# Kernel tuning notes

Measured on AMD Instinct MI355X. Metric: run time of the kernel, lower is better.

Reference implementation:

```python
import jax, jax.numpy as jnp
import numpy as np

B, C, H, W = 8, 256, 64, 64
EPS = 1e-5


def _mk_conv_bn(key, oc, ic):
    k = jax.random.split(key, 6)
    return dict(
        w=jax.random.normal(k[0], (oc, ic), jnp.float32) * 0.01,  # trunc-normal approx, stddev 0.01
        b=jnp.zeros((oc,), jnp.float32),
        s=jax.random.uniform(k[1], (oc,), jnp.float32, 0.5, 1.5),   # BN scale
        t=jax.random.normal(k[2], (oc,), jnp.float32) * 0.1,        # BN shift
        m=jax.random.normal(k[3], (oc,), jnp.float32) * 0.1,        # BN running mean
        v=jax.random.uniform(k[4], (oc,), jnp.float32, 0.5, 1.5),   # BN running var
    )


def setup_inputs() -> dict:
    key = jax.random.key(0)
    ks = jax.random.split(key, 6)
    d = {"x": jax.random.normal(ks[0], (B, C, H, W), jnp.float32)}
    for i, (oc, ic) in zip([1, 2, 3, 4], [(C // 8, C), (C // 8, C), (C // 2, C), (C, C // 2)]):
        p = _mk_conv_bn(ks[i], oc, ic)
        for name, val in p.items():
            d[f"{name}{i}"] = val
    d["gamma"] = jnp.asarray(0.5, jnp.float32)
    return d


def _cbn(x, w, b, s, t, m, v, relu=True):
    # conv1x1 + BatchNorm(eval) [+ ReLU]; dropout is identity at inference
    y = jnp.einsum('bchw,oc->bohw', x, w) + b[None, :, None, None]
    scale = (s / jnp.sqrt(v + EPS))[None, :, None, None]
    y = (y - m[None, :, None, None]) * scale + t[None, :, None, None]
    return jax.nn.relu(y) if relu else y


def _maxpool2(x):
    b, c, h, w = x.shape
    return x.reshape(b, c, h // 2, 2, w // 2, 2).max(axis=(3, 5))


def reference(x, w1, b1, s1, t1, m1, v1, w2, b2, s2, t2, m2, v2,
              w3, b3, s3, t3, m3, v3, w4, b4, s4, t4, m4, v4, gamma):
    b, c, h, w = x.shape
    f = _maxpool2(_cbn(x, w1, b1, s1, t1, m1, v1))   # (B, C/8, H/2, W/2)
    g = _cbn(x, w2, b2, s2, t2, m2, v2)              # (B, C/8, H, W)
    hh = _maxpool2(_cbn(x, w3, b3, s3, t3, m3, v3))  # (B, C/2, H/2, W/2)
    hw, hw4 = h * w, (h // 2) * (w // 2)
    f = f.reshape(b, c // 8, hw4).transpose(0, 2, 1)  # (B, HW/4, C/8)
    g = g.reshape(b, c // 8, hw)                      # (B, C/8, HW)
    s = jnp.einsum('bnk,bkm->bnm', f, g)              # (B, HW/4, HW)
    beta = jax.nn.softmax(s, axis=1)                  # softmax over dim=1, as in source
    hh = hh.reshape(b, c // 2, hw4)                   # (B, C/2, HW/4)
    o = jnp.einsum('bcn,bnm->bcm', hh, beta).reshape(b, c // 2, h, w)
    out = _cbn(o, w4, b4, s4, t4, m4, v4, relu=False)
    return gamma * out + x
```

## Files before the change

### kernel.cpp

```cpp
#include <hip/hip_runtime.h>
#include <hip/hip_bf16.h>

#define HW   4096
#define HW4  1024
#define EPS  1e-5f

typedef __attribute__((ext_vector_type(8))) short bf16x8;
typedef __attribute__((ext_vector_type(4))) float f32x4;

__device__ __forceinline__ short f2bs(float f) {
    union { float f; unsigned u; } v; v.f = f;
    unsigned r = v.u + 0x7FFFu + ((v.u >> 16) & 1u);
    return (short)(r >> 16);
}
__device__ __forceinline__ int swz64(int r, int c)  { return (r << 6) + ((c ^ (r & 7))  << 3); }
__device__ __forceinline__ int swz32(int r, int c)  { return (r << 5) + ((c ^ (r & 3))  << 3); }
__device__ __forceinline__ int swz128(int r, int c) { return (r << 7) + ((c ^ (r & 15)) << 3); }

__global__ __launch_bounds__(256) void conv123pool(
    const float* __restrict__ x,
    const float* __restrict__ w1, const float* __restrict__ b1, const float* __restrict__ s1,
    const float* __restrict__ t1, const float* __restrict__ m1, const float* __restrict__ v1,
    const float* __restrict__ w2, const float* __restrict__ b2, const float* __restrict__ s2,
    const float* __restrict__ t2, const float* __restrict__ m2, const float* __restrict__ v2,
    const float* __restrict__ w3, const float* __restrict__ b3, const float* __restrict__ s3,
    const float* __restrict__ t3, const float* __restrict__ m3, const float* __restrict__ v3,
    short* __restrict__ gbuf, short* __restrict__ fbuf, short* __restrict__ hhbuf)
{
    __shared__ __align__(16) short Wl[64 * 64];
    __shared__ __align__(16) short Xl[128 * 64];
    __shared__ float alB[64], beB[64];

    const int t = threadIdx.x;
    const int lane = t & 63, wv = t >> 6;
    const int quad = lane >> 4, l16 = lane & 15;
    const int ptile = blockIdx.x;
    const int octile = blockIdx.y;
    const int bz = blockIdx.z;
    const int pBase = ptile * 128;

    if (t < 64) {
        int j = octile * 64 + t;
        float pb, ps, ptv, pm, pv;
        if (j < 32)      { pb = b1[j]; ps = s1[j]; ptv = t1[j]; pm = m1[j]; pv = v1[j]; }
        else if (j < 64) { int c = j - 32; pb = b2[c]; ps = s2[c]; ptv = t2[c]; pm = m2[c]; pv = v2[c]; }
        else             { int c = j - 64; pb = b3[c]; ps = s3[c]; ptv = t3[c]; pm = m3[c]; pv = v3[c]; }
        float al = ps * rsqrtf(pv + EPS);
        alB[t] = al; beB[t] = (pb - pm) * al + ptv;
    }

    const f32x4 fzero = {0.f, 0.f, 0.f, 0.f};
    f32x4 acc[8];
    #pragma unroll
    for (int i = 0; i < 8; ++i) acc[i] = fzero;

    const int woc = t >> 2, wkb = (t & 3) * 16;
    const int xp  = t & 127, xk8 = t >> 7;

    for (int k0 = 0; k0 < 256; k0 += 64) {
        {
            int j = octile * 64 + woc;
            const float* wp = (j < 32) ? (w1 + j * 256)
                            : (j < 64) ? (w2 + (j - 32) * 256)
                                       : (w3 + (j - 64) * 256);
            wp += k0 + wkb;
            float4 a = *(const float4*)(wp);
            float4 b = *(const float4*)(wp + 4);
            float4 c = *(const float4*)(wp + 8);
            float4 d = *(const float4*)(wp + 12);
            bf16x8 lo, hi;
            lo[0]=f2bs(a.x); lo[1]=f2bs(a.y); lo[2]=f2bs(a.z); lo[3]=f2bs(a.w);
            lo[4]=f2bs(b.x); lo[5]=f2bs(b.y); lo[6]=f2bs(b.z); lo[7]=f2bs(b.w);
            hi[0]=f2bs(c.x); hi[1]=f2bs(c.y); hi[2]=f2bs(c.z); hi[3]=f2bs(c.w);
            hi[4]=f2bs(d.x); hi[5]=f2bs(d.y); hi[6]=f2bs(d.z); hi[7]=f2bs(d.w);
            *(bf16x8*)&Wl[swz64(woc, (wkb >> 3))]     = lo;
            *(bf16x8*)&Wl[swz64(woc, (wkb >> 3) + 1)] = hi;
        }
        {
            const float* xp0 = x + ((size_t)bz * 256 + k0 + xk8 * 32) * HW + pBase + xp;
            float fv[32];
            #pragma unroll
            for (int i = 0; i < 32; ++i) fv[i] = xp0[(size_t)i * HW];
            #pragma unroll
            for (int c = 0; c < 4; ++c) {
                bf16x8 v;
                #pragma unroll
                for (int jj = 0; jj < 8; ++jj) v[jj] = f2bs(fv[c * 8 + jj]);
                *(bf16x8*)&Xl[swz64(xp, xk8 * 4 + c)] = v;
            }
        }
        __syncthreads();
        #pragma unroll
        for (int kk = 0; kk < 2; ++kk) {
            bf16x8 afr = *(const bf16x8*)&Wl[swz64(wv * 16 + l16, kk * 4 + quad)];
            #pragma unroll
            for (int pt = 0; pt < 8; ++pt) {
                bf16x8 bfr = *(const bf16x8*)&Xl[swz64(pt * 16 + l16, kk * 4 + quad)];
                acc[pt] = __builtin_amdgcn_mfma_f32_16x16x32_bf16(afr, bfr, acc[pt], 0, 0, 0);
            }
        }
        __syncthreads();
    }

    const bool isG = (octile == 0) && (wv >= 2);
    #pragma unroll
    for (int r = 0; r < 4; ++r) {
        int ocl = wv * 16 + quad * 4 + r;
        float al = alB[ocl], be = beB[ocl];
        float y[8];
        #pragma unroll
        for (int pt = 0; pt < 8; ++pt) y[pt] = fmaxf(acc[pt][r] * al + be, 0.f);
        int j = octile * 64 + ocl;
        if (isG) {
            #pragma unroll
            for (int pt = 0; pt < 8; ++pt)
                gbuf[((size_t)bz * 32 + (j - 32)) * HW + pBase + pt * 16 + l16] = f2bs(y[pt]);
        } else {
            #pragma unroll
            for (int pt = 0; pt < 4; ++pt) {
                float v  = fmaxf(y[pt], y[pt + 4]);
                float po = fmaxf(v, __shfl_xor(v, 1));
                if ((l16 & 1) == 0) {
                    int n = ptile * 32 + ((pt * 16 + l16) >> 1);
                    if (j < 32) fbuf[((size_t)bz * 32 + j) * HW4 + n] = f2bs(po);
                    else        hhbuf[((size_t)bz * 128 + (j - 64)) * HW4 + n] = f2bs(po);
                }
            }
        }
    }
}

__global__ __launch_bounds__(256) void attn_conv4(
    const short* __restrict__ gbuf,
    const short* __restrict__ fbuf,
    const short* __restrict__ hhbuf,
    const float* __restrict__ x,
    const float* __restrict__ w4, const float* __restrict__ b4, const float* __restrict__ s4,
    const float* __restrict__ t4, const float* __restrict__ m4, const float* __restrict__ v4,
    const float* __restrict__ gamma, float* __restrict__ out)
{
    __shared__ __align__(16) short smem[24576];
    __shared__ float alB4[256], beB4[256];
    short* gTl = smem;
    short* fTl = smem + 2048;
    short* sTl = smem + 4096;
    short* hhl = smem + 8192;
    short* o_l = smem;
    short* Wl4 = smem + 8192;

    const int t = threadIdx.x;
    const int lane = t & 63, wv = t >> 6;
    const int quad = lane >> 4, l16 = lane & 15;
    const int bz = blockIdx.y;
    const int m0 = blockIdx.x * 64;
    const int ms = wv * 16;
    const f32x4 fzero = {0.f, 0.f, 0.f, 0.f};

    {
        float al = s4[t] * rsqrtf(v4[t] + EPS);
        alB4[t] = al; beB4[t] = (b4[t] - m4[t]) * al + t4[t];
    }

    {
        int mm = t & 63, k8 = t >> 6;
        bf16x8 v;
        #pragma unroll
        for (int j = 0; j < 8; ++j)
            v[j] = gbuf[((size_t)bz * 32 + k8 * 8 + j) * HW + m0 + mm];
        *(bf16x8*)&gTl[swz32(mm, k8)] = v;
    }
    __syncthreads();
    bf16x8 bg = *(const bf16x8*)&gTl[swz32(ms + l16, quad)];

    float runmax = -1e30f, runsum = 0.f;
    f32x4 oacc[8];
    #pragma unroll
    for (int i = 0; i < 8; ++i) oacc[i] = fzero;

    for (int n0 = 0; n0 < 1024; n0 += 64) {
        __syncthreads();
        {
            int nn = t & 63, k8 = t >> 6;
            bf16x8 v;
            #pragma unroll
            for (int j = 0; j < 8; ++j)
                v[j] = fbuf[((size_t)bz * 32 + k8 * 8 + j) * HW4 + n0 + nn];
            *(bf16x8*)&fTl[swz32(nn, k8)] = v;
        }
        {
            int c0 = t >> 3, nc = t & 7;
            #pragma unroll
            for (int i = 0; i < 4; ++i) {
                int c = i * 32 + c0;
                bf16x8 v = *(const bf16x8*)(hhbuf + ((size_t)bz * 128 + c) * HW4 + n0 + nc * 8);
                *(bf16x8*)&hhl[swz64(c, nc)] = v;
            }
        }
        __syncthreads();

        f32x4 sacc[4];
        #pragma unroll
        for (int nt = 0; nt < 4; ++nt) {
            bf16x8 af = *(const bf16x8*)&fTl[swz32(nt * 16 + l16, quad)];
            sacc[nt] = __builtin_amdgcn_mfma_f32_16x16x32_bf16(af, bg, fzero, 0, 0, 0);
        }

        float tmax = -1e30f;
        #pragma unroll
        for (int nt = 0; nt < 4; ++nt)
            #pragma unroll
            for (int r = 0; r < 4; ++r) tmax = fmaxf(tmax, sacc[nt][r]);
        tmax = fmaxf(tmax, __shfl_xor(tmax, 16));
        tmax = fmaxf(tmax, __shfl_xor(tmax, 32));
        float nmax  = fmaxf(runmax, tmax);
        float alpha = __expf(runmax - nmax);
        float psum = 0.f;
        #pragma unroll
        for (int nt = 0; nt < 4; ++nt) {
            short4 ev;
            #pragma unroll
            for (int r = 0; r < 4; ++r) {
                float e = __expf(sacc[nt][r] - nmax);
                psum += e;
                ((short*)&ev)[r] = f2bs(e);
            }
            int chunk = nt * 2 + (quad >> 1);
            *(short4*)&sTl[swz64(ms + l16, chunk) + (quad & 1) * 4] = ev;
        }
        psum += __shfl_xor(psum, 16);
        psum += __shfl_xor(psum, 32);
        runsum = runsum * alpha + psum;
        runmax = nmax;

        #pragma unroll
        for (int ct = 0; ct < 8; ++ct) oacc[ct] = oacc[ct] * alpha;
        #pragma unroll
        for (int kk = 0; kk < 2; ++kk) {
            bf16x8 bs = *(const bf16x8*)&sTl[swz64(ms + l16, kk * 4 + quad)];
            #pragma unroll
            for (int ct = 0; ct < 8; ++ct) {
                bf16x8 ah = *(const bf16x8*)&hhl[swz64(ct * 16 + l16, kk * 4 + quad)];
                oacc[ct] = __builtin_amdgcn_mfma_f32_16x16x32_bf16(ah, bs, oacc[ct], 0, 0, 0);
            }
        }
    }
    __syncthreads();

    {
        float inv = 1.0f / runsum;
        int m = ms + l16;
        #pragma unroll
        for (int ct = 0; ct < 8; ++ct) {
            short4 ov;
            #pragma unroll
            for (int r = 0; r < 4; ++r) ((short*)&ov)[r] = f2bs(oacc[ct][r] * inv);
            *(short4*)&o_l[swz128(m, ct * 2 + (quad >> 1)) + (quad & 1) * 4] = ov;
        }
    }
    __syncthreads();

    f32x4 acc4[4][4];
    #pragma unroll
    for (int i = 0; i < 4; ++i)
        #pragma unroll
        for (int j = 0; j < 4; ++j) acc4[i][j] = fzero;

    for (int c0 = 0; c0 < 128; c0 += 64) {
        #pragma unroll
        for (int i = 0; i < 4; ++i) {
            int oc = i * 64 + (t >> 2);
            int kb = (t & 3) * 16;
            const float* wp = w4 + oc * 128 + c0 + kb;
            float4 a = *(const float4*)(wp);
            float4 b = *(const float4*)(wp + 4);
            float4 c = *(const float4*)(wp + 8);
            float4 d = *(const float4*)(wp + 12);
            bf16x8 lo, hi;
            lo[0]=f2bs(a.x); lo[1]=f2bs(a.y); lo[2]=f2bs(a.z); lo[3]=f2bs(a.w);
            lo[4]=f2bs(b.x); lo[5]=f2bs(b.y); lo[6]=f2bs(b.z); lo[7]=f2bs(b.w);
            hi[0]=f2bs(c.x); hi[1]=f2bs(c.y); hi[2]=f2bs(c.z); hi[3]=f2bs(c.w);
            hi[4]=f2bs(d.x); hi[5]=f2bs(d.y); hi[6]=f2bs(d.z); hi[7]=f2bs(d.w);
            *(bf16x8*)&Wl4[swz64(oc, (kb >> 3))]     = lo;
            *(bf16x8*)&Wl4[swz64(oc, (kb >> 3) + 1)] = hi;
        }
        __syncthreads();
        #pragma unroll
        for (int kk = 0; kk < 2; ++kk) {
            bf16x8 bfr[4];
            #pragma unroll
            for (int mt = 0; mt < 4; ++mt)
                bfr[mt] = *(const bf16x8*)&o_l[swz128(mt * 16 + l16, (c0 >> 3) + kk * 4 + quad)];
            #pragma unroll
            for (int ot = 0; ot < 4; ++ot) {
                bf16x8 afr = *(const bf16x8*)&Wl4[swz64(wv * 64 + ot * 16 + l16, kk * 4 + quad)];
                #pragma unroll
                for (int mt = 0; mt < 4; ++mt)
                    acc4[ot][mt] = __builtin_amdgcn_mfma_f32_16x16x32_bf16(afr, bfr[mt], acc4[ot][mt], 0, 0, 0);
            }
        }
        __syncthreads();
    }

    float gm = gamma[0];
    #pragma unroll
    for (int ot = 0; ot < 4; ++ot) {
        #pragma unroll
        for (int r = 0; r < 4; ++r) {
            int oc = wv * 64 + ot * 16 + quad * 4 + r;
            float al = alB4[oc], be = beB4[oc];
            #pragma unroll
            for (int mt = 0; mt < 4; ++mt) {
                int p = m0 + mt * 16 + l16;
                float y  = acc4[ot][mt][r] * al + be;
                float xo = x[((size_t)bz * 256 + oc) * HW + p];
                out[((size_t)bz * 256 + oc) * HW + p] = gm * y + xo;
            }
        }
    }
}

extern "C" void kernel_launch(void* const* d_in, const int* in_sizes, int n_in,
                              void* d_out, int out_size, void* d_ws, size_t ws_size,
                              hipStream_t stream)
{
    const float* x  = (const float*)d_in[0];
    const float* w1 = (const float*)d_in[1];
    const float* b1 = (const float*)d_in[2];
    const float* s1 = (const float*)d_in[3];
    const float* t1 = (const float*)d_in[4];
    const float* m1 = (const float*)d_in[5];
    const float* v1 = (const float*)d_in[6];
    const float* w2 = (const float*)d_in[7];
    const float* b2 = (const float*)d_in[8];
    const float* s2 = (const float*)d_in[9];
    const float* t2 = (const float*)d_in[10];
    const float* m2 = (const float*)d_in[11];
    const float* v2 = (const float*)d_in[12];
    const float* w3 = (const float*)d_in[13];
    const float* b3 = (const float*)d_in[14];
    const float* s3 = (const float*)d_in[15];
    const float* t3 = (const float*)d_in[16];
    const float* m3 = (const float*)d_in[17];
    const float* v3 = (const float*)d_in[18];
    const float* w4 = (const float*)d_in[19];
    const float* b4 = (const float*)d_in[20];
    const float* s4 = (const float*)d_in[21];
    const float* t4 = (const float*)d_in[22];
    const float* m4 = (const float*)d_in[23];
    const float* v4 = (const float*)d_in[24];
    const float* gm = (const float*)d_in[25];
    float* out = (float*)d_out;

    short* gbuf  = (short*)d_ws;
    short* fbuf  = gbuf  + (size_t)8 * 32 * 4096;
    short* hhbuf = fbuf  + (size_t)8 * 32 * 1024;

    conv123pool<<<dim3(32, 3, 8), 256, 0, stream>>>(
        x, w1, b1, s1, t1, m1, v1, w2, b2, s2, t2, m2, v2, w3, b3, s3, t3, m3, v3,
        gbuf, fbuf, hhbuf);
    attn_conv4<<<dim3(64, 8), 256, 0, stream>>>(
        gbuf, fbuf, hhbuf, x, w4, b4, s4, t4, m4, v4, gm, out);
}
```

Baseline: 173.9 us.

## Fuse conv output-channel tiles per block and prefetch attention tiles into registers

conv123pool now computes all 192 output channels of conv1/2/3 in one block, so each x tile is loaded and converted to bf16 once instead of three times. The grid shrinks from 768 to 256 blocks, trading less parallelism for that reuse. attn_conv4 software-pipelines the f and hh tile loads by prefetching the next tile into registers while the current one is computed. It also swaps the 32-wide XOR swizzle for a padded stride-40 LDS layout and drops one barrier before the conv4 stage.

```diff
diff --git a/kernel.cpp b/kernel.cpp
--- a/kernel.cpp
+++ b/kernel.cpp
@@ -14,8 +14,8 @@
     return (short)(r >> 16);
 }
 __device__ __forceinline__ int swz64(int r, int c)  { return (r << 6) + ((c ^ (r & 7))  << 3); }
-__device__ __forceinline__ int swz32(int r, int c)  { return (r << 5) + ((c ^ (r & 3))  << 3); }
 __device__ __forceinline__ int swz128(int r, int c) { return (r << 7) + ((c ^ (r & 15)) << 3); }
+__device__ __forceinline__ int p40(int r, int c)    { return r * 40 + c * 8; }
 
 __global__ __launch_bounds__(256) void conv123pool(
     const float* __restrict__ x,
@@ -27,43 +27,45 @@
     const float* __restrict__ t3, const float* __restrict__ m3, const float* __restrict__ v3,
     short* __restrict__ gbuf, short* __restrict__ fbuf, short* __restrict__ hhbuf)
 {
-    __shared__ __align__(16) short Wl[64 * 64];
+    __shared__ __align__(16) short Wl[192 * 64];
     __shared__ __align__(16) short Xl[128 * 64];
-    __shared__ float alB[64], beB[64];
+    __shared__ float alB[192], beB[192];
 
     const int t = threadIdx.x;
     const int lane = t & 63, wv = t >> 6;
     const int quad = lane >> 4, l16 = lane & 15;
     const int ptile = blockIdx.x;
-    const int octile = blockIdx.y;
-    const int bz = blockIdx.z;
+    const int bz = blockIdx.y;
     const int pBase = ptile * 128;
 
-    if (t < 64) {
-        int j = octile * 64 + t;
+    if (t < 192) {
+        int j = t;
         float pb, ps, ptv, pm, pv;
         if (j < 32)      { pb = b1[j]; ps = s1[j]; ptv = t1[j]; pm = m1[j]; pv = v1[j]; }
         else if (j < 64) { int c = j - 32; pb = b2[c]; ps = s2[c]; ptv = t2[c]; pm = m2[c]; pv = v2[c]; }
         else             { int c = j - 64; pb = b3[c]; ps = s3[c]; ptv = t3[c]; pm = m3[c]; pv = v3[c]; }
         float al = ps * rsqrtf(pv + EPS);
-        alB[t] = al; beB[t] = (pb - pm) * al + ptv;
+        alB[j] = al; beB[j] = (pb - pm) * al + ptv;
     }
 
     const f32x4 fzero = {0.f, 0.f, 0.f, 0.f};
-    f32x4 acc[8];
-    #pragma unroll
-    for (int i = 0; i < 8; ++i) acc[i] = fzero;
-
-    const int woc = t >> 2, wkb = (t & 3) * 16;
+    f32x4 acc[3][8];
+    #pragma unroll
+    for (int i = 0; i < 3; ++i)
+        #pragma unroll
+        for (int j = 0; j < 8; ++j) acc[i][j] = fzero;
+
     const int xp  = t & 127, xk8 = t >> 7;
 
     for (int k0 = 0; k0 < 256; k0 += 64) {
-        {
-            int j = octile * 64 + woc;
-            const float* wp = (j < 32) ? (w1 + j * 256)
-                            : (j < 64) ? (w2 + (j - 32) * 256)
-                                       : (w3 + (j - 64) * 256);
-            wp += k0 + wkb;
+        #pragma unroll
+        for (int i = 0; i < 3; ++i) {
+            int idx = t + i * 256;
+            int oc = idx >> 2, kb = (idx & 3) * 16;
+            const float* wp = (oc < 32) ? (w1 + oc * 256)
+                            : (oc < 64) ? (w2 + (oc - 32) * 256)
+                                        : (w3 + (oc - 64) * 256);
+            wp += k0 + kb;
             float4 a = *(const float4*)(wp);
             float4 b = *(const float4*)(wp + 4);
             float4 c = *(const float4*)(wp + 8);
@@ -73,8 +75,8 @@
             lo[4]=f2bs(b.x); lo[5]=f2bs(b.y); lo[6]=f2bs(b.z); lo[7]=f2bs(b.w);
             hi[0]=f2bs(c.x); hi[1]=f2bs(c.y); hi[2]=f2bs(c.z); hi[3]=f2bs(c.w);
             hi[4]=f2bs(d.x); hi[5]=f2bs(d.y); hi[6]=f2bs(d.z); hi[7]=f2bs(d.w);
-            *(bf16x8*)&Wl[swz64(woc, (wkb >> 3))]     = lo;
-            *(bf16x8*)&Wl[swz64(woc, (wkb >> 3) + 1)] = hi;
+            *(bf16x8*)&Wl[swz64(oc, (kb >> 3))]     = lo;
+            *(bf16x8*)&Wl[swz64(oc, (kb >> 3) + 1)] = hi;
         }
         {
             const float* xp0 = x + ((size_t)bz * 256 + k0 + xk8 * 32) * HW + pBase + xp;
@@ -92,38 +94,44 @@
         __syncthreads();
         #pragma unroll
         for (int kk = 0; kk < 2; ++kk) {
-            bf16x8 afr = *(const bf16x8*)&Wl[swz64(wv * 16 + l16, kk * 4 + quad)];
-            #pragma unroll
-            for (int pt = 0; pt < 8; ++pt) {
-                bf16x8 bfr = *(const bf16x8*)&Xl[swz64(pt * 16 + l16, kk * 4 + quad)];
-                acc[pt] = __builtin_amdgcn_mfma_f32_16x16x32_bf16(afr, bfr, acc[pt], 0, 0, 0);
-            }
-        }
-        __syncthreads();
-    }
-
-    const bool isG = (octile == 0) && (wv >= 2);
-    #pragma unroll
-    for (int r = 0; r < 4; ++r) {
-        int ocl = wv * 16 + quad * 4 + r;
-        float al = alB[ocl], be = beB[ocl];
-        float y[8];
-        #pragma unroll
-        for (int pt = 0; pt < 8; ++pt) y[pt] = fmaxf(acc[pt][r] * al + be, 0.f);
-        int j = octile * 64 + ocl;
-        if (isG) {
+            bf16x8 bfr[8];
             #pragma unroll
             for (int pt = 0; pt < 8; ++pt)
-                gbuf[((size_t)bz * 32 + (j - 32)) * HW + pBase + pt * 16 + l16] = f2bs(y[pt]);
-        } else {
-            #pragma unroll
-            for (int pt = 0; pt < 4; ++pt) {
-                float v  = fmaxf(y[pt], y[pt + 4]);
-                float po = fmaxf(v, __shfl_xor(v, 1));
-                if ((l16 & 1) == 0) {
-                    int n = ptile * 32 + ((pt * 16 + l16) >> 1);
-                    if (j < 32) fbuf[((size_t)bz * 32 + j) * HW4 + n] = f2bs(po);
-                    else        hhbuf[((size_t)bz * 128 + (j - 64)) * HW4 + n] = f2bs(po);
+                bfr[pt] = *(const bf16x8*)&Xl[swz64(pt * 16 + l16, kk * 4 + quad)];
+            #pragma unroll
+            for (int tt = 0; tt < 3; ++tt) {
+                bf16x8 afr = *(const bf16x8*)&Wl[swz64(wv * 48 + tt * 16 + l16, kk * 4 + quad)];
+                #pragma unroll
+                for (int pt = 0; pt < 8; ++pt)
+                    acc[tt][pt] = __builtin_amdgcn_mfma_f32_16x16x32_bf16(afr, bfr[pt], acc[tt][pt], 0, 0, 0);
+            }
+        }
+        __syncthreads();
+    }
+
+    #pragma unroll
+    for (int tt = 0; tt < 3; ++tt) {
+        #pragma unroll
+        for (int r = 0; r < 4; ++r) {
+            int j = wv * 48 + tt * 16 + quad * 4 + r;
+            float al = alB[j], be = beB[j];
+            float y[8];
+            #pragma unroll
+            for (int pt = 0; pt < 8; ++pt) y[pt] = fmaxf(acc[tt][pt][r] * al + be, 0.f);
+            if (j >= 32 && j < 64) {
+                #pragma unroll
+                for (int pt = 0; pt < 8; ++pt)
+                    gbuf[((size_t)bz * 32 + (j - 32)) * HW + pBase + pt * 16 + l16] = f2bs(y[pt]);
+            } else {
+                #pragma unroll
+                for (int pt = 0; pt < 4; ++pt) {
+                    float v  = fmaxf(y[pt], y[pt + 4]);
+                    float po = fmaxf(v, __shfl_xor(v, 1));
+                    if ((l16 & 1) == 0) {
+                        int n = ptile * 32 + ((pt * 16 + l16) >> 1);
+                        if (j < 32) fbuf[((size_t)bz * 32 + j) * HW4 + n] = f2bs(po);
+                        else        hhbuf[((size_t)bz * 128 + (j - 64)) * HW4 + n] = f2bs(po);
+                    }
                 }
             }
         }
@@ -139,14 +147,14 @@
     const float* __restrict__ t4, const float* __restrict__ m4, const float* __restrict__ v4,
     const float* __restrict__ gamma, float* __restrict__ out)
 {
-    __shared__ __align__(16) short smem[24576];
+    __shared__ __align__(16) short smem[25600];
     __shared__ float alB4[256], beB4[256];
     short* gTl = smem;
-    short* fTl = smem + 2048;
-    short* sTl = smem + 4096;
-    short* hhl = smem + 8192;
+    short* fTl = smem + 2560;
+    short* sTl = smem + 5120;
+    short* hhl = smem + 9216;
     short* o_l = smem;
-    short* Wl4 = smem + 8192;
+    short* Wl4 = smem + 9216;
 
     const int t = threadIdx.x;
     const int lane = t & 63, wv = t >> 6;
@@ -167,10 +175,24 @@
         #pragma unroll
         for (int j = 0; j < 8; ++j)
             v[j] = gbuf[((size_t)bz * 32 + k8 * 8 + j) * HW + m0 + mm];
-        *(bf16x8*)&gTl[swz32(mm, k8)] = v;
-    }
+        *(bf16x8*)&gTl[p40(mm, k8)] = v;
+    }
+
+    const int fnn = t & 63, fk8 = t >> 6;
+    const int hc0 = t >> 3, hnc = t & 7;
+    const short* fB = fbuf + (size_t)bz * 32 * HW4;
+    const short* hB = hhbuf + (size_t)bz * 128 * HW4;
+    unsigned short fpre[8];
+    bf16x8 hpre[4];
+    #pragma unroll
+    for (int j = 0; j < 8; ++j)
+        fpre[j] = (unsigned short)fB[(fk8 * 8 + j) * HW4 + fnn];
+    #pragma unroll
+    for (int i = 0; i < 4; ++i)
+        hpre[i] = *(const bf16x8*)(hB + (size_t)(i * 32 + hc0) * HW4 + hnc * 8);
+
     __syncthreads();
-    bf16x8 bg = *(const bf16x8*)&gTl[swz32(ms + l16, quad)];
+    bf16x8 bg = *(const bf16x8*)&gTl[p40(ms + l16, quad)];
 
     float runmax = -1e30f, runsum = 0.f;
     f32x4 oacc[8];
@@ -180,28 +202,29 @@
     for (int n0 = 0; n0 < 1024; n0 += 64) {
         __syncthreads();
         {
-            int nn = t & 63, k8 = t >> 6;
             bf16x8 v;
             #pragma unroll
+            for (int j = 0; j < 8; ++j) v[j] = (short)fpre[j];
+            *(bf16x8*)&fTl[p40(fnn, fk8)] = v;
+            #pragma unroll
+            for (int i = 0; i < 4; ++i)
+                *(bf16x8*)&hhl[swz64(i * 32 + hc0, hnc)] = hpre[i];
+        }
+        __syncthreads();
+        if (n0 + 64 < 1024) {
+            int n1 = n0 + 64;
+            #pragma unroll
             for (int j = 0; j < 8; ++j)
-                v[j] = fbuf[((size_t)bz * 32 + k8 * 8 + j) * HW4 + n0 + nn];
-            *(bf16x8*)&fTl[swz32(nn, k8)] = v;
-        }
-        {
-            int c0 = t >> 3, nc = t & 7;
-            #pragma unroll
-            for (int i = 0; i < 4; ++i) {
-                int c = i * 32 + c0;
-                bf16x8 v = *(const bf16x8*)(hhbuf + ((size_t)bz * 128 + c) * HW4 + n0 + nc * 8);
-                *(bf16x8*)&hhl[swz64(c, nc)] = v;
-            }
-        }
-        __syncthreads();
+                fpre[j] = (unsigned short)fB[(fk8 * 8 + j) * HW4 + n1 + fnn];
+            #pragma unroll
+            for (int i = 0; i < 4; ++i)
+                hpre[i] = *(const bf16x8*)(hB + (size_t)(i * 32 + hc0) * HW4 + n1 + hnc * 8);
+        }
 
         f32x4 sacc[4];
         #pragma unroll
         for (int nt = 0; nt < 4; ++nt) {
-            bf16x8 af = *(const bf16x8*)&fTl[swz32(nt * 16 + l16, quad)];
+            bf16x8 af = *(const bf16x8*)&fTl[p40(nt * 16 + l16, quad)];
             sacc[nt] = __builtin_amdgcn_mfma_f32_16x16x32_bf16(af, bg, fzero, 0, 0, 0);
         }
 
@@ -257,7 +280,6 @@
             *(short4*)&o_l[swz128(m, ct * 2 + (quad >> 1)) + (quad & 1) * 4] = ov;
         }
     }
-    __syncthreads();
 
     f32x4 acc4[4][4];
     #pragma unroll
@@ -355,7 +377,7 @@
     short* fbuf  = gbuf  + (size_t)8 * 32 * 4096;
     short* hhbuf = fbuf  + (size_t)8 * 32 * 1024;
 
-    conv123pool<<<dim3(32, 3, 8), 256, 0, stream>>>(
+    conv123pool<<<dim3(32, 8), 256, 0, stream>>>(
         x, w1, b1, s1, t1, m1, v1, w2, b2, s2, t2, m2, v2, w3, b3, s3, t3, m3, v3,
         gbuf, fbuf, hhbuf);
     attn_conv4<<<dim3(64, 8), 256, 0, stream>>>(
```

New measurement: 180.7 us. 1.04x slower.
